# Performance work log

Hardware: AMD Instinct MI355X
Metric: run time of the kernel (lower is better)

## Reference

```python
import jax, jax.numpy as jnp
import numpy as np

V, E, H = 32000, 128, 128   # vocab, embed, hidden
B, T = 32, 128              # batch, seq_len
NEG = -1e9


def setup_inputs() -> dict:
    key = jax.random.key(0)
    ks = jax.random.split(key, 11)
    return {
        "x": jax.random.randint(ks[0], (B, T), 0, V),
        "embedding": jax.random.normal(ks[1], (V, E), jnp.float32) * 0.1,
        "W_ih": jax.random.normal(ks[2], (E, 3 * H), jnp.float32) * 0.1,
        "W_hh": jax.random.normal(ks[3], (H, 3 * H), jnp.float32) * 0.1,
        "b": jnp.zeros((3 * H,), jnp.float32),
        "attn_w": jax.random.normal(ks[4], (H, H), jnp.float32) * (1.0 / np.sqrt(H)),
        "attn_b": jnp.zeros((H,), jnp.float32),
        "v_w": jax.random.normal(ks[5], (H, 1), jnp.float32) * (1.0 / np.sqrt(H)),
        "v_b": jnp.zeros((1,), jnp.float32),
        "fc_w": jax.random.normal(ks[6], (2 * H, V), jnp.float32) * (1.0 / np.sqrt(2 * H)),
        "fc_b": jnp.zeros((V,), jnp.float32),
    }


def _forward(x, embedding, W_ih, W_hh, b, attn_w, attn_b, v_w, v_b, fc_w, fc_b):
    Bx, Tx = x.shape
    emb = embedding[x]                      # (B,T,E)
    xg = emb @ W_ih + b                     # (B,T,3H) precomputed input gates

    def step(h, xg_t):
        gates = xg_t + h @ W_hh             # (B,3H)
        i_z, i_r, i_n = jnp.split(gates, 3, axis=-1)
        z = jax.nn.sigmoid(i_z)
        r = jax.nn.sigmoid(i_r)
        n = jnp.tanh(i_n * r)               # NOTE: original multiplies r into i_n
        h_new = (1.0 - z) * n + z * h
        return h_new, h_new

    h0 = jnp.zeros((Bx, W_hh.shape[0]), dtype=emb.dtype)
    _, hs = jax.lax.scan(step, h0, jnp.swapaxes(xg, 0, 1))  # (T,B,H)
    hs = jnp.swapaxes(hs, 0, 1)             # (B,T,H)

    # Bahdanau-style scores on each hidden state (independent of query step)
    scores = (jnp.tanh(hs @ attn_w + attn_b) @ v_w + v_b)[..., 0]  # (B,T)
    # at step t, attend over h_0..h_{t-1} (strictly before t)
    q = jnp.arange(Tx)
    mask = q[:, None] > q[None, :]          # (T,T): key < query
    masked = jnp.where(mask[None], scores[:, None, :], NEG)
    w = jax.nn.softmax(masked, axis=-1) * mask[None]  # row t=0 zeroed -> context 0
    context = jnp.einsum('bts,bsh->bth', w, hs)       # (B,T,H)

    combined = jnp.concatenate([hs, context], axis=-1)  # (B,T,2H)
    return combined @ fc_w + fc_b            # (B,T,V)


def reference(x, embedding, W_ih, W_hh, b, attn_w, attn_b, v_w, v_b, fc_w, fc_b):
    return _forward(x, embedding, W_ih, W_hh, b, attn_w, attn_b, v_w, v_b, fc_w, fc_b)
```

## Files before the change

kernel.cpp:

```cpp
#include <hip/hip_runtime.h>

typedef _Float16 f16;
typedef _Float16 f16x8 __attribute__((ext_vector_type(8)));
typedef float    f32x4 __attribute__((ext_vector_type(4)));

#define V  32000
#define E  128
#define H  128
#define B  32
#define T  128
#define G3 384

__global__ __launch_bounds__(256) void k0_convert_fcw(const float* __restrict__ fc_w,
                                                      f16* __restrict__ Bt16)
{
    int v  = blockIdx.x * 256 + threadIdx.x;
    int k0 = blockIdx.y * 64;
    for (int kk = 0; kk < 64; kk += 8) {
        f16x8 p;
        #pragma unroll
        for (int e = 0; e < 8; ++e)
            p[e] = (f16)fc_w[(size_t)(k0 + kk + e) * V + v];
        *(f16x8*)(Bt16 + (size_t)v * 256 + (k0 + kk)) = p;
    }
}

__global__ __launch_bounds__(384) void k1_embed_xg(const int* __restrict__ x,
                                                   const float* __restrict__ emb,
                                                   const float* __restrict__ W_ih,
                                                   const float* __restrict__ bias,
                                                   float* __restrict__ xg)
{
    int j = threadIdx.x;
    float w[E];
    #pragma unroll
    for (int k = 0; k < E; ++k) w[k] = W_ih[k * G3 + j];
    float bj = bias[j];

    __shared__ __align__(16) float erow[16][E];
    int row0 = blockIdx.x * 16;
    for (int i = j; i < 16 * E; i += G3) {
        int r = i >> 7, c = i & (E - 1);
        erow[r][c] = emb[(size_t)x[row0 + r] * E + c];
    }
    __syncthreads();
    for (int r = 0; r < 16; ++r) {
        float acc = bj;
        #pragma unroll
        for (int k = 0; k < E; k += 4) {
            f32x4 hv = *(const f32x4*)&erow[r][k];
            acc += hv[0]*w[k] + hv[1]*w[k+1] + hv[2]*w[k+2] + hv[3]*w[k+3];
        }
        xg[(size_t)(row0 + r) * G3 + j] = acc;
    }
}

__global__ __launch_bounds__(384) void k2_gru(const float* __restrict__ xg,
                                              const float* __restrict__ W_hh,
                                              float* __restrict__ hs,
                                              f16* __restrict__ A16)
{
    int b = blockIdx.x;
    int j = threadIdx.x;
    float w[H];
    #pragma unroll
    for (int k = 0; k < H; ++k) w[k] = W_hh[k * G3 + j];

    __shared__ __align__(16) float h[H];
    __shared__ float g[G3];
    if (j < H) h[j] = 0.0f;
    __syncthreads();

    const float* xgb = xg + (size_t)b * T * G3;
    float xnext = xgb[j];
    for (int t = 0; t < T; ++t) {
        float s0 = xnext, s1 = 0.f, s2 = 0.f, s3 = 0.f;
        if (t + 1 < T) xnext = xgb[(size_t)(t + 1) * G3 + j];
        #pragma unroll
        for (int k = 0; k < H; k += 16) {
            f32x4 h0 = *(const f32x4*)&h[k];
            f32x4 h1 = *(const f32x4*)&h[k + 4];
            f32x4 h2 = *(const f32x4*)&h[k + 8];
            f32x4 h3 = *(const f32x4*)&h[k + 12];
            s0 += h0[0]*w[k]    + h0[1]*w[k+1]  + h0[2]*w[k+2]  + h0[3]*w[k+3];
            s1 += h1[0]*w[k+4]  + h1[1]*w[k+5]  + h1[2]*w[k+6]  + h1[3]*w[k+7];
            s2 += h2[0]*w[k+8]  + h2[1]*w[k+9]  + h2[2]*w[k+10] + h2[3]*w[k+11];
            s3 += h3[0]*w[k+12] + h3[1]*w[k+13] + h3[2]*w[k+14] + h3[3]*w[k+15];
        }
        g[j] = (s0 + s1) + (s2 + s3);
        __syncthreads();
        if (j < H) {
            float z  = 1.0f / (1.0f + __expf(-g[j]));
            float r  = 1.0f / (1.0f + __expf(-g[H + j]));
            float pn = g[2 * H + j] * r;
            float ex = __expf(2.0f * pn);
            float n  = 1.0f - 2.0f / (ex + 1.0f);
            float hn = (1.0f - z) * n + z * h[j];
            h[j] = hn;
            size_t bt = (size_t)b * T + t;
            hs[bt * H + j] = hn;
            A16[bt * 256 + j] = (f16)hn;
        }
        __syncthreads();
    }
}

__global__ __launch_bounds__(128) void k3_scores(const float* __restrict__ hs,
                                                 const float* __restrict__ attn_w,
                                                 const float* __restrict__ attn_b,
                                                 const float* __restrict__ v_w,
                                                 const float* __restrict__ v_b,
                                                 float* __restrict__ scores)
{
    int i = threadIdx.x;
    float w[H];
    #pragma unroll
    for (int k = 0; k < H; ++k) w[k] = attn_w[k * H + i];
    float ab = attn_b[i];
    float vw = v_w[i];
    float vb = v_b[0];

    __shared__ __align__(16) float hrow[H];
    __shared__ float part[2];
    int row0 = blockIdx.x * 16;
    for (int r = 0; r < 16; ++r) {
        hrow[i] = hs[(size_t)(row0 + r) * H + i];
        __syncthreads();
        float acc = ab;
        #pragma unroll
        for (int k = 0; k < H; k += 4) {
            f32x4 hv = *(const f32x4*)&hrow[k];
            acc += hv[0]*w[k] + hv[1]*w[k+1] + hv[2]*w[k+2] + hv[3]*w[k+3];
        }
        float ex = __expf(2.0f * acc);
        float u  = (1.0f - 2.0f / (ex + 1.0f)) * vw;
        #pragma unroll
        for (int o = 32; o > 0; o >>= 1) u += __shfl_xor(u, o);
        if ((i & 63) == 0) part[i >> 6] = u;
        __syncthreads();
        if (i == 0) scores[row0 + r] = part[0] + part[1] + vb;
        __syncthreads();
    }
}

__global__ __launch_bounds__(128) void k4_context(const float* __restrict__ hs,
                                                  const float* __restrict__ scores,
                                                  f16* __restrict__ A16)
{
    int bt = blockIdx.x;
    int b  = bt >> 7;
    int t  = bt & (T - 1);
    int i  = threadIdx.x;

    __shared__ float wts[T];
    __shared__ float redm[2], reds[2];
    const float* sc = scores + b * T;

    float sv = (i < t) ? sc[i] : -3.0e38f;
    float m = sv;
    #pragma unroll
    for (int o = 32; o > 0; o >>= 1) m = fmaxf(m, __shfl_xor(m, o));
    if ((i & 63) == 0) redm[i >> 6] = m;
    __syncthreads();
    m = fmaxf(redm[0], redm[1]);

    float ev = (i < t) ? __expf(sc[i] - m) : 0.0f;
    float s = ev;
    #pragma unroll
    for (int o = 32; o > 0; o >>= 1) s += __shfl_xor(s, o);
    if ((i & 63) == 0) reds[i >> 6] = s;
    __syncthreads();
    s = reds[0] + reds[1];

    float inv = (t > 0) ? 1.0f / s : 0.0f;
    wts[i] = ev * inv;
    __syncthreads();

    float ctx = 0.0f;
    const float* hsb = hs + (size_t)b * T * H + i;
    for (int sI = 0; sI < t; ++sI)
        ctx = fmaf(wts[sI], hsb[(size_t)sI * H], ctx);

    A16[(size_t)bt * 256 + H + i] = (f16)ctx;
}

__global__ __launch_bounds__(512, 4) void k5_gemm(const f16* __restrict__ A16,
                                                  const f16* __restrict__ Bt16,
                                                  const float* __restrict__ fc_b,
                                                  float* __restrict__ out)
{
    __shared__ __align__(16) char Bs[2][32768];
    int mi   = blockIdx.x;
    int ni   = blockIdx.y;
    int tid  = threadIdx.x;
    int w    = tid >> 6;
    int lane = tid & 63;
    int l15  = lane & 15;
    int lhi  = lane >> 4;

    const f16* Ab = A16 + (size_t)(mi * 128 + w * 16 + l15) * 256 + lhi * 8;
    f16x8 a[8];
    #pragma unroll
    for (int kt = 0; kt < 8; ++kt)
        a[kt] = *(const f16x8*)(Ab + kt * 32);

#define STAGE(cc, buf)                                                          \
    {                                                                           \
        const char* src = (const char*)(Bt16 + (size_t)(cc) * 64 * 256);        \
        _Pragma("unroll")                                                       \
        for (int it = 0; it < 4; ++it) {                                        \
            int ck  = it * 8 + w;                                               \
            int lin = ck * 1024 + lane * 16;                                    \
            int row = lin >> 9;                                                 \
            int g   = lin ^ ((row & 7) << 4);                                   \
            __builtin_amdgcn_global_load_lds(                                   \
                (const __attribute__((address_space(1))) void*)(src + g),       \
                (__attribute__((address_space(3))) void*)(&Bs[buf][0] + ck * 1024), \
                16, 0, 0);                                                      \
        }                                                                       \
    }

    STAGE(ni, 0);
    asm volatile("s_waitcnt vmcnt(0)");
    __syncthreads();

    int nc = (500 - ni + 15) >> 4;
    for (int j = 0; j < nc; ++j) {
        int c   = ni + j * 16;
        int cur = j & 1;

        if (j + 1 < nc) STAGE(c + 16, cur ^ 1);
        __builtin_amdgcn_sched_barrier(0);

        f32x4 acc[4];
        #pragma unroll
        for (int f = 0; f < 4; ++f)
            acc[f] = *(const f32x4*)(fc_b + c * 64 + f * 16 + lhi * 4);

        const char* bb = &Bs[cur][0];
        #pragma unroll
        for (int kt = 0; kt < 8; ++kt) {
            f16x8 bf[4];
            #pragma unroll
            for (int f = 0; f < 4; ++f) {
                int r  = f * 16 + l15;
                int ad = r * 512 + ((kt * 64 + lhi * 16) ^ ((r & 7) << 4));
                bf[f] = *(const f16x8*)(bb + ad);
            }
            #pragma unroll
            for (int f = 0; f < 4; ++f)
                acc[f] = __builtin_amdgcn_mfma_f32_16x16x32_f16(bf[f], a[kt], acc[f], 0, 0, 0);
        }

        int row = mi * 128 + w * 16 + l15;
        #pragma unroll
        for (int f = 0; f < 4; ++f)
            *(f32x4*)(out + (size_t)row * V + c * 64 + f * 16 + lhi * 4) = acc[f];

        if (j + 1 < nc) {
            __builtin_amdgcn_sched_barrier(0);
            asm volatile("s_waitcnt vmcnt(4)" ::: "memory");
            __builtin_amdgcn_s_barrier();
            __builtin_amdgcn_sched_barrier(0);
        }
    }
#undef STAGE
}

extern "C" void kernel_launch(void* const* d_in, const int* in_sizes, int n_in,
                              void* d_out, int out_size, void* d_ws, size_t ws_size,
                              hipStream_t stream)
{
    (void)in_sizes; (void)n_in; (void)out_size; (void)ws_size;
    const int*   x      = (const int*)  d_in[0];
    const float* emb    = (const float*)d_in[1];
    const float* W_ih   = (const float*)d_in[2];
    const float* W_hh   = (const float*)d_in[3];
    const float* bias   = (const float*)d_in[4];
    const float* attn_w = (const float*)d_in[5];
    const float* attn_b = (const float*)d_in[6];
    const float* v_w    = (const float*)d_in[7];
    const float* v_b    = (const float*)d_in[8];
    const float* fc_w   = (const float*)d_in[9];
    const float* fc_b   = (const float*)d_in[10];
    float* out = (float*)d_out;

    char* ws = (char*)d_ws;
    float* xg     = (float*)(ws);
    float* hs     = (float*)(ws + 6291456);
    float* scores = (float*)(ws + 8388608);
    f16*   A16    = (f16*)  (ws + 8404992);
    f16*   Bt16   = (f16*)  (ws + 10502144);

    hipLaunchKernelGGL(k0_convert_fcw, dim3(V / 256, 4), dim3(256), 0, stream, fc_w, Bt16);
    hipLaunchKernelGGL(k1_embed_xg,    dim3(B * T / 16), dim3(G3),  0, stream, x, emb, W_ih, bias, xg);
    hipLaunchKernelGGL(k2_gru,         dim3(B),          dim3(G3),  0, stream, xg, W_hh, hs, A16);
    hipLaunchKernelGGL(k3_scores,      dim3(B * T / 16), dim3(H),   0, stream, hs, attn_w, attn_b, v_w, v_b, scores);
    hipLaunchKernelGGL(k4_context,     dim3(B * T),      dim3(H),   0, stream, hs, scores, A16);
    hipLaunchKernelGGL(k5_gemm,        dim3(32, 16),     dim3(512), 0, stream, A16, Bt16, fc_b, out);
}
```

Measured before the change: 392.8 us.

## Fuse attention scores and context into GRU kernel; remap GEMM block order

The GRU recurrence kernel now also computes the Bahdanau score for the previous hidden state inside each time step, reusing the h vector already in LDS. It keeps all hidden states in shared memory and, after the scan, computes the masked softmax and context per time step, writing directly into the fp16 GEMM input. This removes two kernel launches and the global round trips for hs and scores. The price is extra per-thread registers (a second 128-float column) and 64KB of LDS in a 32-block kernel that sits on the critical path. The GEMM launch also moves to a 1D grid with a swizzled mapping of blocks to tiles, which changes cache locality.

```diff
diff --git a/kernel.cpp b/kernel.cpp
--- a/kernel.cpp
+++ b/kernel.cpp
@@ -1,6 +1,7 @@
 #include <hip/hip_runtime.h>
 
 typedef _Float16 f16;
+typedef _Float16 f16x2 __attribute__((ext_vector_type(2)));
 typedef _Float16 f16x8 __attribute__((ext_vector_type(8)));
 typedef float    f32x4 __attribute__((ext_vector_type(4)));
 
@@ -55,19 +56,38 @@
     }
 }
 
-__global__ __launch_bounds__(384) void k2_gru(const float* __restrict__ xg,
-                                              const float* __restrict__ W_hh,
-                                              float* __restrict__ hs,
-                                              f16* __restrict__ A16)
-{
-    int b = blockIdx.x;
-    int j = threadIdx.x;
+__global__ __launch_bounds__(384) void kseq(const float* __restrict__ xg,
+                                            const float* __restrict__ W_hh,
+                                            const float* __restrict__ attn_w,
+                                            const float* __restrict__ attn_b,
+                                            const float* __restrict__ v_w,
+                                            const float* __restrict__ v_b,
+                                            f16* __restrict__ A16)
+{
+    int b    = blockIdx.x;
+    int j    = threadIdx.x;
+    int lane = j & 63;
+    int wv   = j >> 6;
+
     float w[H];
     #pragma unroll
     for (int k = 0; k < H; ++k) w[k] = W_hh[k * G3 + j];
 
+    float acol[H];
+    float ab = 0.f, vwgt = 0.f;
+    if (j < H) {
+        #pragma unroll
+        for (int k = 0; k < H; ++k) acol[k] = attn_w[k * H + j];
+        ab = attn_b[j];
+        vwgt = v_w[j];
+    }
+    float vb = v_b[0];
+
     __shared__ __align__(16) float h[H];
     __shared__ float g[G3];
+    __shared__ float part[2];
+    __shared__ float sc_lds[T];
+    __shared__ __align__(16) float hs_lds[T][H];
     if (j < H) h[j] = 0.0f;
     __syncthreads();
 
@@ -75,6 +95,7 @@
     float xnext = xgb[j];
     for (int t = 0; t < T; ++t) {
         float s0 = xnext, s1 = 0.f, s2 = 0.f, s3 = 0.f;
+        float sc0 = 0.f, sc1 = 0.f;
         if (t + 1 < T) xnext = xgb[(size_t)(t + 1) * G3 + j];
         #pragma unroll
         for (int k = 0; k < H; k += 16) {
@@ -86,8 +107,22 @@
             s1 += h1[0]*w[k+4]  + h1[1]*w[k+5]  + h1[2]*w[k+6]  + h1[3]*w[k+7];
             s2 += h2[0]*w[k+8]  + h2[1]*w[k+9]  + h2[2]*w[k+10] + h2[3]*w[k+11];
             s3 += h3[0]*w[k+12] + h3[1]*w[k+13] + h3[2]*w[k+14] + h3[3]*w[k+15];
+            if (j < H) {
+                sc0 += h0[0]*acol[k]    + h0[1]*acol[k+1]  + h0[2]*acol[k+2]  + h0[3]*acol[k+3]
+                     + h1[0]*acol[k+4]  + h1[1]*acol[k+5]  + h1[2]*acol[k+6]  + h1[3]*acol[k+7];
+                sc1 += h2[0]*acol[k+8]  + h2[1]*acol[k+9]  + h2[2]*acol[k+10] + h2[3]*acol[k+11]
+                     + h3[0]*acol[k+12] + h3[1]*acol[k+13] + h3[2]*acol[k+14] + h3[3]*acol[k+15];
+            }
         }
         g[j] = (s0 + s1) + (s2 + s3);
+        if (j < H && t > 0) {
+            float sc = sc0 + sc1 + ab;
+            float ex = __expf(2.0f * sc);
+            float u  = (1.0f - 2.0f / (ex + 1.0f)) * vwgt;
+            #pragma unroll
+            for (int o = 32; o > 0; o >>= 1) u += __shfl_xor(u, o);
+            if (lane == 0) part[wv] = u;
+        }
         __syncthreads();
         if (j < H) {
             float z  = 1.0f / (1.0f + __expf(-g[j]));
@@ -97,91 +132,35 @@
             float n  = 1.0f - 2.0f / (ex + 1.0f);
             float hn = (1.0f - z) * n + z * h[j];
             h[j] = hn;
-            size_t bt = (size_t)b * T + t;
-            hs[bt * H + j] = hn;
-            A16[bt * 256 + j] = (f16)hn;
-        }
+            hs_lds[t][j] = hn;
+            A16[((size_t)b * T + t) * 256 + j] = (f16)hn;
+        }
+        if (j == 0 && t > 0) sc_lds[t - 1] = part[0] + part[1] + vb;
         __syncthreads();
     }
-}
-
-__global__ __launch_bounds__(128) void k3_scores(const float* __restrict__ hs,
-                                                 const float* __restrict__ attn_w,
-                                                 const float* __restrict__ attn_b,
-                                                 const float* __restrict__ v_w,
-                                                 const float* __restrict__ v_b,
-                                                 float* __restrict__ scores)
-{
-    int i = threadIdx.x;
-    float w[H];
-    #pragma unroll
-    for (int k = 0; k < H; ++k) w[k] = attn_w[k * H + i];
-    float ab = attn_b[i];
-    float vw = v_w[i];
-    float vb = v_b[0];
-
-    __shared__ __align__(16) float hrow[H];
-    __shared__ float part[2];
-    int row0 = blockIdx.x * 16;
-    for (int r = 0; r < 16; ++r) {
-        hrow[i] = hs[(size_t)(row0 + r) * H + i];
-        __syncthreads();
-        float acc = ab;
-        #pragma unroll
-        for (int k = 0; k < H; k += 4) {
-            f32x4 hv = *(const f32x4*)&hrow[k];
-            acc += hv[0]*w[k] + hv[1]*w[k+1] + hv[2]*w[k+2] + hv[3]*w[k+3];
-        }
-        float ex = __expf(2.0f * acc);
-        float u  = (1.0f - 2.0f / (ex + 1.0f)) * vw;
-        #pragma unroll
-        for (int o = 32; o > 0; o >>= 1) u += __shfl_xor(u, o);
-        if ((i & 63) == 0) part[i >> 6] = u;
-        __syncthreads();
-        if (i == 0) scores[row0 + r] = part[0] + part[1] + vb;
-        __syncthreads();
-    }
-}
-
-__global__ __launch_bounds__(128) void k4_context(const float* __restrict__ hs,
-                                                  const float* __restrict__ scores,
-                                                  f16* __restrict__ A16)
-{
-    int bt = blockIdx.x;
-    int b  = bt >> 7;
-    int t  = bt & (T - 1);
-    int i  = threadIdx.x;
-
-    __shared__ float wts[T];
-    __shared__ float redm[2], reds[2];
-    const float* sc = scores + b * T;
-
-    float sv = (i < t) ? sc[i] : -3.0e38f;
-    float m = sv;
-    #pragma unroll
-    for (int o = 32; o > 0; o >>= 1) m = fmaxf(m, __shfl_xor(m, o));
-    if ((i & 63) == 0) redm[i >> 6] = m;
-    __syncthreads();
-    m = fmaxf(redm[0], redm[1]);
-
-    float ev = (i < t) ? __expf(sc[i] - m) : 0.0f;
-    float s = ev;
-    #pragma unroll
-    for (int o = 32; o > 0; o >>= 1) s += __shfl_xor(s, o);
-    if ((i & 63) == 0) reds[i >> 6] = s;
-    __syncthreads();
-    s = reds[0] + reds[1];
-
-    float inv = (t > 0) ? 1.0f / s : 0.0f;
-    wts[i] = ev * inv;
-    __syncthreads();
-
-    float ctx = 0.0f;
-    const float* hsb = hs + (size_t)b * T * H + i;
-    for (int sI = 0; sI < t; ++sI)
-        ctx = fmaf(wts[sI], hsb[(size_t)sI * H], ctx);
-
-    A16[(size_t)bt * 256 + H + i] = (f16)ctx;
+
+    for (int t = wv; t < T; t += 6) {
+        float sv0 = (lane < t)      ? sc_lds[lane]      : -3.0e38f;
+        float sv1 = (lane + 64 < t) ? sc_lds[lane + 64] : -3.0e38f;
+        float m = fmaxf(sv0, sv1);
+        #pragma unroll
+        for (int o = 32; o > 0; o >>= 1) m = fmaxf(m, __shfl_xor(m, o));
+        float ee = ((lane < t)      ? __expf(sv0 - m) : 0.f)
+                 + ((lane + 64 < t) ? __expf(sv1 - m) : 0.f);
+        #pragma unroll
+        for (int o = 32; o > 0; o >>= 1) ee += __shfl_xor(ee, o);
+        float inv = (t > 0) ? 1.0f / ee : 0.0f;
+
+        float c0 = 0.f, c1 = 0.f;
+        for (int s = 0; s < t; ++s) {
+            float ws = __expf(sc_lds[s] - m) * inv;
+            float2 hv = *(const float2*)&hs_lds[s][lane * 2];
+            c0 = fmaf(ws, hv.x, c0);
+            c1 = fmaf(ws, hv.y, c1);
+        }
+        f16x2 o2 = { (f16)c0, (f16)c1 };
+        *(f16x2*)(A16 + ((size_t)b * T + t) * 256 + H + lane * 2) = o2;
+    }
 }
 
 __global__ __launch_bounds__(512, 4) void k5_gemm(const f16* __restrict__ A16,
@@ -190,8 +169,9 @@
                                                   float* __restrict__ out)
 {
     __shared__ __align__(16) char Bs[2][32768];
-    int mi   = blockIdx.x;
-    int ni   = blockIdx.y;
+    int bid  = blockIdx.x;
+    int ni   = ((bid & 7) << 1) | (bid >> 8);
+    int mi   = (bid >> 3) & 31;
     int tid  = threadIdx.x;
     int w    = tid >> 6;
     int lane = tid & 63;
@@ -287,15 +267,12 @@
 
     char* ws = (char*)d_ws;
     float* xg     = (float*)(ws);
-    float* hs     = (float*)(ws + 6291456);
-    float* scores = (float*)(ws + 8388608);
     f16*   A16    = (f16*)  (ws + 8404992);
     f16*   Bt16   = (f16*)  (ws + 10502144);
 
     hipLaunchKernelGGL(k0_convert_fcw, dim3(V / 256, 4), dim3(256), 0, stream, fc_w, Bt16);
     hipLaunchKernelGGL(k1_embed_xg,    dim3(B * T / 16), dim3(G3),  0, stream, x, emb, W_ih, bias, xg);
-    hipLaunchKernelGGL(k2_gru,         dim3(B),          dim3(G3),  0, stream, xg, W_hh, hs, A16);
-    hipLaunchKernelGGL(k3_scores,      dim3(B * T / 16), dim3(H),   0, stream, hs, attn_w, attn_b, v_w, v_b, scores);
-    hipLaunchKernelGGL(k4_context,     dim3(B * T),      dim3(H),   0, stream, hs, scores, A16);
-    hipLaunchKernelGGL(k5_gemm,        dim3(32, 16),     dim3(512), 0, stream, A16, Bt16, fc_b, out);
-}
+    hipLaunchKernelGGL(kseq,           dim3(B),          dim3(G3),  0, stream,
+                       xg, W_hh, attn_w, attn_b, v_w, v_b, A16);
+    hipLaunchKernelGGL(k5_gemm,        dim3(512),        dim3(512), 0, stream, A16, Bt16, fc_b, out);
+}
```

After: 1.253 ms. 219% more time.
